# Kernel tuning notes

Measured on AMD Instinct MI355X. Metric: run time of the kernel, lower is better.

The kernel has to match this reference:

```python
import jax, jax.numpy as jnp
import numpy as np

B_, L_, D_, E_, N_, DT_, K_ = 2, 1024, 1024, 2048, 16, 64, 4
EPS = 1e-5


def setup_inputs() -> dict:
    key = jax.random.key(0)
    ks = jax.random.split(key, 16)
    s = lambda *sh: 1.0 / np.sqrt(sh[-1])
    return {
        "resid": jax.random.normal(ks[0], (B_, L_, D_), jnp.float32),
        "norm_w": jnp.ones((D_,), jnp.float32),
        "skip_w": jax.random.normal(ks[1], (E_, D_), jnp.float32) * s(E_, D_),
        "in_w": jax.random.normal(ks[2], (E_, D_), jnp.float32) * s(E_, D_),
        "conv_w": jax.random.normal(ks[3], (E_, K_), jnp.float32) * s(E_, K_),
        "conv_b": jax.random.normal(ks[4], (E_,), jnp.float32) * 0.1,
        "wd1": jax.random.normal(ks[5], (DT_, E_), jnp.float32) * s(DT_, E_),
        "wd2": jax.random.normal(ks[6], (E_, DT_), jnp.float32) * s(E_, DT_),
        "wd2_b": jax.random.normal(ks[7], (E_,), jnp.float32) * 0.1,
        "wb": jax.random.normal(ks[8], (N_, E_), jnp.float32) * s(N_, E_),
        "wc": jax.random.normal(ks[9], (N_, E_), jnp.float32) * s(N_, E_),
        "A_log": jnp.log(jax.random.uniform(ks[10], (E_, N_), jnp.float32, 0.5, 4.0)),
        "W_D": jnp.ones((E_,), jnp.float32),
        "out_w": jax.random.normal(ks[11], (D_, E_), jnp.float32) * s(D_, E_),
    }


def _forward(resid, norm_w, skip_w, in_w, conv_w, conv_b, wd1, wd2, wd2_b,
             wb, wc, A_log, W_D, out_w):
    B, L, D = resid.shape
    E, N = A_log.shape
    K = conv_w.shape[-1]
    # RMSNorm
    xn = resid * jax.lax.rsqrt(jnp.mean(resid * resid, -1, keepdims=True) + EPS) * norm_w
    skip = jnp.einsum('bld,ed->ble', xn, skip_w)
    x = jnp.einsum('bld,ed->ble', xn, in_w)
    # causal depthwise conv1d (torch pads both sides by K-1, output cut to [:L])
    xp = jnp.pad(x, ((0, 0), (K - 1, 0), (0, 0)))
    conv = conv_b + sum(xp[:, k:k + L, :] * conv_w[:, k] for k in range(K))
    x = jax.nn.silu(conv)  # [B,L,E] ssm input
    # input-dependent projections
    delta = jax.nn.softplus(jnp.einsum('ble,re->blr', x, wd1) @ wd2.T + wd2_b)  # [B,L,E]
    Bt = jnp.einsum('ble,ne->bln', x, wb)  # [B,L,N]
    Ct = jnp.einsum('ble,ne->bln', x, wc)  # [B,L,N]
    A = -jnp.exp(A_log)  # [E,N]

    def step(h, inp):
        dt, b_t, c_t, x_t = inp  # [B,E],[B,N],[B,N],[B,E]
        A_bar = jnp.exp(dt[:, :, None] * A)          # [B,E,N]
        h = A_bar * h + (dt * x_t)[:, :, None] * b_t[:, None, :]
        y = jnp.einsum('ben,bn->be', h, c_t)
        return h, y

    h0 = jnp.zeros((B, E, N), x.dtype)
    xs = (delta.transpose(1, 0, 2), Bt.transpose(1, 0, 2),
          Ct.transpose(1, 0, 2), x.transpose(1, 0, 2))
    _, y = jax.lax.scan(step, h0, xs)
    y = y.transpose(1, 0, 2)  # [B,L,E]
    y = y + x * W_D
    y = y * jax.nn.silu(skip)
    y = jnp.einsum('ble,de->bld', y, out_w)
    return resid + y


def reference(resid, norm_w, skip_w, in_w, conv_w, conv_b, wd1, wd2, wd2_b,
              wb, wc, A_log, W_D, out_w):
    return _forward(resid, norm_w, skip_w, in_w, conv_w, conv_b, wd1, wd2,
                    wd2_b, wb, wc, A_log, W_D, out_w)
```

## Files before the change

### kernel.cpp

```cpp
#include <hip/hip_runtime.h>
#include <cstdint>

typedef unsigned short u16;
typedef float f32x4 __attribute__((ext_vector_type(4)));
typedef __bf16 bf16x8 __attribute__((ext_vector_type(8)));
typedef u16 u16x8 __attribute__((ext_vector_type(8)));

__device__ __forceinline__ u16 f2bf(float f) {
  uint32_t u = __float_as_uint(f);
  u += 0x7fffu + ((u >> 16) & 1u);
  return (u16)(u >> 16);
}
__device__ __forceinline__ float bf2f(u16 s) {
  return __uint_as_float(((uint32_t)s) << 16);
}

__device__ __forceinline__ void ld16(const u16* g, u16* l) {
  auto* gp = reinterpret_cast<const __attribute__((address_space(1))) u16*>(
      reinterpret_cast<uintptr_t>(g));
  auto* lp = reinterpret_cast<__attribute__((address_space(3))) u16*>(
      static_cast<uint32_t>(reinterpret_cast<uintptr_t>(l)));
  __builtin_amdgcn_global_load_lds(gp, lp, 16, 0, 0);
}

__device__ __forceinline__ f32x4 mfma16(u16x8 a, u16x8 b, f32x4 c) {
  return __builtin_amdgcn_mfma_f32_16x16x32_bf16(
      __builtin_bit_cast(bf16x8, a), __builtin_bit_cast(bf16x8, b), c, 0, 0, 0);
}

__device__ __forceinline__ float sigmoidf_(float x) { return 1.f / (1.f + __expf(-x)); }
__device__ __forceinline__ float siluf_(float x) { return x * sigmoidf_(x); }
__device__ __forceinline__ float softplusf_(float x) {
  return fmaxf(x, 0.f) + log1pf(__expf(-fabsf(x)));
}

#define PACK_TOT 6651904
__global__ __launch_bounds__(256) void pack_rms_kernel(
    const float* __restrict__ skip_w, const float* __restrict__ in_w,
    const float* __restrict__ out_w, const float* __restrict__ wd2,
    const float* __restrict__ wd1, const float* __restrict__ wb,
    const float* __restrict__ wc, const float* __restrict__ A_log,
    u16* __restrict__ skipw_bf, u16* __restrict__ inw_bf, u16* __restrict__ outw_bf,
    u16* __restrict__ wd2_bf, u16* __restrict__ w96, float* __restrict__ Aneg,
    const float* __restrict__ resid, const float* __restrict__ norm_w,
    u16* __restrict__ xn_bf) {
  int t = threadIdx.x;
  if (blockIdx.x >= 1024) {
    int row = blockIdx.x - 1024;
    const float4* xr = (const float4*)(resid + (size_t)row * 1024);
    float4 v = xr[t];
    float ss = v.x * v.x + v.y * v.y + v.z * v.z + v.w * v.w;
    for (int o = 32; o > 0; o >>= 1) ss += __shfl_xor(ss, o);
    __shared__ float wsum[4];
    if ((t & 63) == 0) wsum[t >> 6] = ss;
    __syncthreads();
    float tot = wsum[0] + wsum[1] + wsum[2] + wsum[3];
    float rs = rsqrtf(tot * (1.0f / 1024.0f) + 1e-5f);
    float4 wv = ((const float4*)norm_w)[t];
    uint2 pk;
    pk.x = (uint32_t)f2bf(v.x * rs * wv.x) | ((uint32_t)f2bf(v.y * rs * wv.y) << 16);
    pk.y = (uint32_t)f2bf(v.z * rs * wv.z) | ((uint32_t)f2bf(v.w * rs * wv.w) << 16);
    ((uint2*)xn_bf)[row * 256 + t] = pk;
    return;
  }
  const int stride = 1024 * 256;
  for (int i = blockIdx.x * 256 + t; i < PACK_TOT; i += stride) {
    int j = i;
    if (j < 2097152) { skipw_bf[j] = f2bf(skip_w[j]); continue; } j -= 2097152;
    if (j < 2097152) { inw_bf[j] = f2bf(in_w[j]); continue; } j -= 2097152;
    if (j < 2097152) { outw_bf[j] = f2bf(out_w[j]); continue; } j -= 2097152;
    if (j < 131072)  { wd2_bf[j] = f2bf(wd2[j]); continue; } j -= 131072;
    if (j < 131072)  { w96[j] = f2bf(wd1[j]); continue; } j -= 131072;
    if (j < 32768)   { w96[131072 + j] = f2bf(wb[j]); continue; } j -= 32768;
    if (j < 32768)   { w96[163840 + j] = f2bf(wc[j]); continue; } j -= 32768;
    Aneg[j] = -__expf(A_log[j]);
  }
}

template <int BM, int BN, int BK, int EPI>
__global__ __launch_bounds__(256) void gemm_bt(
    const u16* __restrict__ A, const u16* __restrict__ B0, const u16* __restrict__ B1,
    int M, int N, int K, int Nsplit,
    void* __restrict__ C0, void* __restrict__ C1,
    const float* __restrict__ addsrc) {
  constexpr int TM = BM / 32, TN = BN / 32;
  constexpr int KC = BK / 8;
  __shared__ __align__(16) u16 sA[BM * BK];
  __shared__ __align__(16) u16 sB[BN * BK];
  const int t = threadIdx.x;
  const int lane = t & 63, wid = t >> 6;
  const int wm = wid >> 1, wn = wid & 1;
  const int mBase = blockIdx.y * BM;
  const int nBase = blockIdx.x * BN;
  const bool hi = (nBase >= Nsplit);
  const u16* Bp = hi ? B1 : B0;
  const int nB0 = nBase - (hi ? Nsplit : 0);
  const int col = lane & 15, quad = lane >> 4;

  f32x4 acc[TM][TN];
#pragma unroll
  for (int i = 0; i < TM; ++i)
#pragma unroll
    for (int j = 0; j < TN; ++j) acc[i][j] = f32x4{0.f, 0.f, 0.f, 0.f};

  for (int k0 = 0; k0 < K; k0 += BK) {
#pragma unroll
    for (int c = t; c < BM * KC; c += 256) {
      int row = c / KC, j = c % KC;
      int k8 = ((j + row) & (KC - 1)) * 8;
      ld16(A + (size_t)(mBase + row) * K + k0 + k8, &sA[c * 8]);
    }
#pragma unroll
    for (int c = t; c < BN * KC; c += 256) {
      int row = c / KC, j = c % KC;
      int k8 = ((j + row) & (KC - 1)) * 8;
      ld16(Bp + (size_t)(nB0 + row) * K + k0 + k8, &sB[c * 8]);
    }
    __syncthreads();
#pragma unroll
    for (int kk = 0; kk < BK / 32; ++kk) {
      u16x8 af[TM], bfv[TN];
#pragma unroll
      for (int i = 0; i < TM; ++i) {
        int rowA = wm * (BM / 2) + i * 16 + col;
        af[i] = *(const u16x8*)&sA[rowA * BK + (((kk * 4 + quad) - rowA) & (KC - 1)) * 8];
      }
#pragma unroll
      for (int j = 0; j < TN; ++j) {
        int rowB = wn * (BN / 2) + j * 16 + col;
        bfv[j] = *(const u16x8*)&sB[rowB * BK + (((kk * 4 + quad) - rowB) & (KC - 1)) * 8];
      }
#pragma unroll
      for (int i = 0; i < TM; ++i)
#pragma unroll
        for (int j = 0; j < TN; ++j) acc[i][j] = mfma16(af[i], bfv[j], acc[i][j]);
    }
    __syncthreads();
  }

#pragma unroll
  for (int i = 0; i < TM; ++i) {
#pragma unroll
    for (int j = 0; j < TN; ++j) {
#pragma unroll
      for (int r = 0; r < 4; ++r) {
        int gm = mBase + wm * (BM / 2) + i * 16 + quad * 4 + r;
        int gn = nBase + wn * (BN / 2) + j * 16 + col;
        float v = acc[i][j][r];
        if (EPI == 0) {
          if (gn < Nsplit)
            ((u16*)C0)[(size_t)gm * Nsplit + gn] = f2bf(v);
          else
            ((u16*)C1)[(size_t)gm * (N - Nsplit) + (gn - Nsplit)] = f2bf(v);
        } else {
          ((float*)C0)[(size_t)gm * N + gn] = addsrc[(size_t)gm * N + gn] + v;
        }
      }
    }
  }
}

__global__ __launch_bounds__(256) void conv_skinny_kernel(
    const u16* __restrict__ xin_bf, const float* __restrict__ conv_w,
    const float* __restrict__ conv_b, u16* __restrict__ xconv_bf,
    const u16* __restrict__ w96, float* __restrict__ dbc) {
  constexpr int PAD = 264;
  __shared__ __align__(16) u16 sA[64 * PAD];
  __shared__ __align__(16) u16 sB[96 * 128];
  const int t = threadIdx.x, lane = t & 63, w = t >> 6;
  const int mBase = blockIdx.x * 64;
  const int e0 = blockIdx.y * 256;

  {
    const int ep = (t & 127) * 2;
    const int strip = t >> 7;
    const int ms = mBase + strip * 32;
    const int l0 = ms & 1023;
    const uint32_t* xr = (const uint32_t*)xin_bf;
    size_t base = ((size_t)ms * 2048 + e0 + ep) >> 1;
    int eg = e0 + ep;
    float4 w0 = ((const float4*)conv_w)[eg];
    float4 w1 = ((const float4*)conv_w)[eg + 1];
    float b0 = conv_b[eg], b1 = conv_b[eg + 1];
    uint32_t u;
    u = (l0 >= 1) ? xr[base - 1024] : 0u;
    float h10 = bf2f((u16)u), h11 = bf2f((u16)(u >> 16));
    u = (l0 >= 2) ? xr[base - 2048] : 0u;
    float h20 = bf2f((u16)u), h21 = bf2f((u16)(u >> 16));
    u = (l0 >= 3) ? xr[base - 3072] : 0u;
    float h30 = bf2f((u16)u), h31 = bf2f((u16)(u >> 16));
#pragma unroll 4
    for (int r = 0; r < 32; ++r) {
      uint32_t ux = xr[base + (size_t)r * 1024];
      float x0 = bf2f((u16)ux), x1 = bf2f((u16)(ux >> 16));
      float a0 = b0 + w0.w * x0 + w0.z * h10 + w0.y * h20 + w0.x * h30;
      float a1 = b1 + w1.w * x1 + w1.z * h11 + w1.y * h21 + w1.x * h31;
      a0 = siluf_(a0); a1 = siluf_(a1);
      uint32_t pk = (uint32_t)f2bf(a0) | ((uint32_t)f2bf(a1) << 16);
      ((uint32_t*)xconv_bf)[base + (size_t)r * 1024] = pk;
      *(uint32_t*)&sA[(strip * 32 + r) * PAD + ep] = pk;
      h30 = h20; h31 = h21; h20 = h10; h21 = h11; h10 = x0; h11 = x1;
    }
  }
  for (int c = t; c < 96 * 16; c += 256) {
    int row = c >> 4, j = c & 15;
    int k8 = ((j + row) & 15) * 8;
    ld16(w96 + (size_t)row * 2048 + e0 + k8, &sB[c * 8]);
  }
  __syncthreads();
  const int col = lane & 15, quad = lane >> 4;
  const int rowA = w * 16 + col;
  f32x4 acc[6];
#pragma unroll
  for (int j = 0; j < 6; ++j) acc[j] = f32x4{0.f, 0.f, 0.f, 0.f};
#pragma unroll
  for (int kk = 0; kk < 4; ++kk) {
    u16x8 af = *(const u16x8*)&sA[rowA * PAD + kk * 32 + quad * 8];
#pragma unroll
    for (int j = 0; j < 6; ++j) {
      int rowB = j * 16 + col;
      u16x8 bfv = *(const u16x8*)&sB[rowB * 128 + (((kk * 4 + quad) - rowB) & 15) * 8];
      acc[j] = mfma16(af, bfv, acc[j]);
    }
  }
  __syncthreads();
  for (int c = t; c < 96 * 16; c += 256) {
    int row = c >> 4, j = c & 15;
    int k8 = ((j + row) & 15) * 8;
    ld16(w96 + (size_t)row * 2048 + e0 + 128 + k8, &sB[c * 8]);
  }
  __syncthreads();
#pragma unroll
  for (int kk = 4; kk < 8; ++kk) {
    u16x8 af = *(const u16x8*)&sA[rowA * PAD + kk * 32 + quad * 8];
#pragma unroll
    for (int j = 0; j < 6; ++j) {
      int rowB = j * 16 + col;
      u16x8 bfv = *(const u16x8*)&sB[rowB * 128 + ((((kk - 4) * 4 + quad) - rowB) & 15) * 8];
      acc[j] = mfma16(af, bfv, acc[j]);
    }
  }
#pragma unroll
  for (int j = 0; j < 6; ++j)
#pragma unroll
    for (int r = 0; r < 4; ++r) {
      int gm = mBase + w * 16 + quad * 4 + r;
      int gn = j * 16 + col;
      atomicAdd(&dbc[gm * 96 + gn], acc[j][r]);
    }
}

__device__ __forceinline__ void delta_tile(
    const float* __restrict__ dbc, const u16* __restrict__ wd2_bf,
    const float* __restrict__ wd2_b, int m0, int e0,
    u16* sD1, float* sDT, float* sBC) {
  const int t = threadIdx.x;
  for (int i = t; i < 2048; i += 256)
    sD1[i] = f2bf(dbc[(m0 + (i >> 6)) * 96 + (i & 63)]);
  for (int j = t; j < 1024; j += 256)
    sBC[j] = dbc[(m0 + (j >> 5)) * 96 + 64 + (j & 31)];
  __syncthreads();
  const int lane = t & 63, wid = t >> 6;
  const int col = lane & 15, quad = lane >> 4;
  const int mt = wid & 1, ntB = (wid >> 1) * 8;
  u16x8 afr0 = *(const u16x8*)&sD1[(mt * 16 + col) * 64 + quad * 8];
  u16x8 afr1 = *(const u16x8*)&sD1[(mt * 16 + col) * 64 + 32 + quad * 8];
#pragma unroll
  for (int jj = 0; jj < 8; ++jj) {
    int ecol = (ntB + jj) * 16 + col;
    int erow = e0 + ecol;
    u16x8 b0 = *(const u16x8*)&wd2_bf[(size_t)erow * 64 + quad * 8];
    u16x8 b1 = *(const u16x8*)&wd2_bf[(size_t)erow * 64 + 32 + quad * 8];
    f32x4 dacc = f32x4{0.f, 0.f, 0.f, 0.f};
    dacc = mfma16(afr0, b0, dacc);
    dacc = mfma16(afr1, b1, dacc);
    float bias = wd2_b[erow];
#pragma unroll
    for (int r = 0; r < 4; ++r)
      sDT[(mt * 16 + quad * 4 + r) * 260 + ecol] = softplusf_(dacc[r] + bias);
  }
  __syncthreads();
}

__global__ __launch_bounds__(256) void scan1_kernel(
    const float* __restrict__ dbc, const u16* __restrict__ wd2_bf,
    const float* __restrict__ wd2_b, const u16* __restrict__ xconv_bf,
    const float* __restrict__ Aneg, float* __restrict__ hloc,
    float* __restrict__ Ssum) {
  __shared__ __align__(16) float sDT[32 * 260];
  __shared__ __align__(16) u16 sD1[32 * 64];
  __shared__ float sBC[1024];
  const int t = threadIdx.x;
  const int eb = blockIdx.x, c = blockIdx.y, b = blockIdx.z;
  const int e0 = eb * 256;
  const int m0 = b * 1024 + c * 32;
  delta_tile(dbc, wd2_bf, wd2_b, m0, e0, sD1, sDT, sBC);
  const int e = e0 + t;
  float Ar[16], h[16];
#pragma unroll
  for (int n = 0; n < 16; ++n) { Ar[n] = Aneg[e * 16 + n]; h[n] = 0.f; }
  float S = 0.f;
  for (int l = 0; l < 32; ++l) {
    size_t m = (size_t)(m0 + l) * 2048 + e;
    float dt = sDT[l * 260 + t];
    float xv = bf2f(xconv_bf[m]);
    S += dt;
    float dx = dt * xv;
    const float* bl = &sBC[l * 32];
#pragma unroll
    for (int n = 0; n < 16; ++n) h[n] = __expf(dt * Ar[n]) * h[n] + dx * bl[n];
  }
  size_t base = ((size_t)(b * 32 + c) * 2048 + e) * 16;
#pragma unroll
  for (int n = 0; n < 16; ++n) hloc[base + n] = h[n];
  Ssum[(b * 32 + c) * 2048 + e] = S;
}

__global__ __launch_bounds__(256) void combine_kernel(
    const float* __restrict__ Aneg, const float* __restrict__ Ssum,
    float* __restrict__ hloc) {
  int tid = blockIdx.x * 256 + threadIdx.x;
  int b = tid >> 15, r = tid & 32767;
  int e = r >> 4;
  float a = Aneg[r];
  float h = 0.f;
  for (int c = 0; c < 32; ++c) {
    size_t base = (size_t)(b * 32 + c) * 32768 + r;
    float hl = hloc[base];
    float S = Ssum[(b * 32 + c) * 2048 + e];
    hloc[base] = h;
    h = __expf(a * S) * h + hl;
  }
}

__global__ __launch_bounds__(256) void scan2_kernel(
    const float* __restrict__ dbc, const u16* __restrict__ wd2_bf,
    const float* __restrict__ wd2_b, const u16* __restrict__ xconv_bf,
    const float* __restrict__ Aneg, const float* __restrict__ hloc,
    const u16* __restrict__ skip_bf, const float* __restrict__ W_D,
    u16* __restrict__ yfin_bf) {
  __shared__ __align__(16) float sDT[32 * 260];
  __shared__ __align__(16) u16 sD1[32 * 64];
  __shared__ float sBC[1024];
  const int t = threadIdx.x;
  const int eb = blockIdx.x, c = blockIdx.y, b = blockIdx.z;
  const int e0 = eb * 256;
  const int m0 = b * 1024 + c * 32;
  delta_tile(dbc, wd2_bf, wd2_b, m0, e0, sD1, sDT, sBC);
  const int e = e0 + t;
  float Ar[16], h[16];
  size_t hbase = ((size_t)(b * 32 + c) * 2048 + e) * 16;
#pragma unroll
  for (int n = 0; n < 16; ++n) { Ar[n] = Aneg[e * 16 + n]; h[n] = hloc[hbase + n]; }
  float wd = W_D[e];
  for (int l = 0; l < 32; ++l) {
    size_t m = (size_t)(m0 + l) * 2048 + e;
    float dt = sDT[l * 260 + t];
    float xv = bf2f(xconv_bf[m]);
    float dx = dt * xv;
    const float* bl = &sBC[l * 32];
    float y = 0.f;
#pragma unroll
    for (int n = 0; n < 16; ++n) {
      h[n] = __expf(dt * Ar[n]) * h[n] + dx * bl[n];
      y += h[n] * bl[16 + n];
    }
    float yv = y + xv * wd;
    float sk = bf2f(skip_bf[m]);
    yv *= sk * sigmoidf_(sk);
    yfin_bf[m] = f2bf(yv);
  }
}

extern "C" void kernel_launch(void* const* d_in, const int* in_sizes, int n_in,
                              void* d_out, int out_size, void* d_ws, size_t ws_size,
                              hipStream_t stream) {
  (void)in_sizes; (void)n_in; (void)out_size; (void)ws_size;
  const float* resid  = (const float*)d_in[0];
  const float* norm_w = (const float*)d_in[1];
  const float* skip_w = (const float*)d_in[2];
  const float* in_w   = (const float*)d_in[3];
  const float* conv_w = (const float*)d_in[4];
  const float* conv_b = (const float*)d_in[5];
  const float* wd1    = (const float*)d_in[6];
  const float* wd2    = (const float*)d_in[7];
  const float* wd2_b  = (const float*)d_in[8];
  const float* wb     = (const float*)d_in[9];
  const float* wc     = (const float*)d_in[10];
  const float* A_log  = (const float*)d_in[11];
  const float* W_D    = (const float*)d_in[12];
  const float* out_w  = (const float*)d_in[13];

  char* p = (char*)d_ws;
  u16*   skipw_bf = (u16*)(p + 0);
  u16*   inw_bf   = (u16*)(p + 4194304);
  u16*   outw_bf  = (u16*)(p + 8388608);
  u16*   wd2_bf   = (u16*)(p + 12582912);
  u16*   w96      = (u16*)(p + 12845056);
  float* Aneg     = (float*)(p + 13238272);
  u16*   xn_bf    = (u16*)(p + 13369344);
  u16*   skip_bf  = (u16*)(p + 17563648);
  u16*   xin_bf   = (u16*)(p + 25952256);
  u16*   xconv_bf = (u16*)(p + 34340864);
  float* dbc      = (float*)(p + 42729472);
  u16*   yfin_bf  = (u16*)(p + 43515904);
  float* hloc     = (float*)(p + 51904512);
  float* Ssum     = (float*)(p + 60293120);

  hipMemsetAsync((void*)dbc, 0, 2048 * 96 * sizeof(float), stream);
  pack_rms_kernel<<<3072, 256, 0, stream>>>(
      skip_w, in_w, out_w, wd2, wd1, wb, wc, A_log,
      skipw_bf, inw_bf, outw_bf, wd2_bf, w96, Aneg,
      resid, norm_w, xn_bf);
  gemm_bt<128, 128, 64, 0><<<dim3(32, 16), 256, 0, stream>>>(
      xn_bf, skipw_bf, inw_bf, 2048, 4096, 1024, 2048,
      (void*)skip_bf, (void*)xin_bf, nullptr);
  conv_skinny_kernel<<<dim3(32, 8), 256, 0, stream>>>(
      xin_bf, conv_w, conv_b, xconv_bf, w96, dbc);
  scan1_kernel<<<dim3(8, 32, 2), 256, 0, stream>>>(
      dbc, wd2_bf, wd2_b, xconv_bf, Aneg, hloc, Ssum);
  combine_kernel<<<256, 256, 0, stream>>>(Aneg, Ssum, hloc);
  scan2_kernel<<<dim3(8, 32, 2), 256, 0, stream>>>(
      dbc, wd2_bf, wd2_b, xconv_bf, Aneg, hloc, skip_bf, W_D, yfin_bf);
  gemm_bt<64, 64, 128, 2><<<dim3(16, 32), 256, 0, stream>>>(
      yfin_bf, outw_bf, outw_bf, 2048, 1024, 2048, 1024,
      (void*)d_out, nullptr, resid);
}
```

Before: 236.3 us.

## Split-K output GEMM with atomics, smaller tiles, and more blocks for conv and combine

The out-projection GEMM is split along K into two halves that accumulate into the output with atomicAdd. The output is pre-seeded with the residual through a device memcpy. The input GEMM uses 128x64 tiles with launch_bounds occupancy 4, giving more blocks. The conv kernel processes 128 channels per block so twice as many blocks launch, and the combine kernel prefetches the next chunk and uses smaller blocks. The aim is to fill more CUs on small grids, at the cost of atomic traffic, non-deterministic summation order and an extra memcpy.

```diff
diff --git a/kernel.cpp b/kernel.cpp
--- a/kernel.cpp
+++ b/kernel.cpp
@@ -78,11 +78,10 @@
 }
 
 template <int BM, int BN, int BK, int EPI>
-__global__ __launch_bounds__(256) void gemm_bt(
+__global__ __launch_bounds__(256, 4) void gemm_bt(
     const u16* __restrict__ A, const u16* __restrict__ B0, const u16* __restrict__ B1,
-    int M, int N, int K, int Nsplit,
-    void* __restrict__ C0, void* __restrict__ C1,
-    const float* __restrict__ addsrc) {
+    int N, int K, int Kld, int mTiles, int Nsplit,
+    void* __restrict__ C0, void* __restrict__ C1) {
   constexpr int TM = BM / 32, TN = BN / 32;
   constexpr int KC = BK / 8;
   __shared__ __align__(16) u16 sA[BM * BK];
@@ -90,7 +89,9 @@
   const int t = threadIdx.x;
   const int lane = t & 63, wid = t >> 6;
   const int wm = wid >> 1, wn = wid & 1;
-  const int mBase = blockIdx.y * BM;
+  const int by = blockIdx.y & (mTiles - 1);
+  const int kOff = (blockIdx.y / mTiles) * K;
+  const int mBase = by * BM;
   const int nBase = blockIdx.x * BN;
   const bool hi = (nBase >= Nsplit);
   const u16* Bp = hi ? B1 : B0;
@@ -103,18 +104,18 @@
 #pragma unroll
     for (int j = 0; j < TN; ++j) acc[i][j] = f32x4{0.f, 0.f, 0.f, 0.f};
 
-  for (int k0 = 0; k0 < K; k0 += BK) {
+  for (int k0 = kOff; k0 < kOff + K; k0 += BK) {
 #pragma unroll
     for (int c = t; c < BM * KC; c += 256) {
       int row = c / KC, j = c % KC;
       int k8 = ((j + row) & (KC - 1)) * 8;
-      ld16(A + (size_t)(mBase + row) * K + k0 + k8, &sA[c * 8]);
+      ld16(A + (size_t)(mBase + row) * Kld + k0 + k8, &sA[c * 8]);
     }
 #pragma unroll
     for (int c = t; c < BN * KC; c += 256) {
       int row = c / KC, j = c % KC;
       int k8 = ((j + row) & (KC - 1)) * 8;
-      ld16(Bp + (size_t)(nB0 + row) * K + k0 + k8, &sB[c * 8]);
+      ld16(Bp + (size_t)(nB0 + row) * Kld + k0 + k8, &sB[c * 8]);
     }
     __syncthreads();
 #pragma unroll
@@ -153,7 +154,7 @@
           else
             ((u16*)C1)[(size_t)gm * (N - Nsplit) + (gn - Nsplit)] = f2bf(v);
         } else {
-          ((float*)C0)[(size_t)gm * N + gn] = addsrc[(size_t)gm * N + gn] + v;
+          atomicAdd(&((float*)C0)[(size_t)gm * N + gn], v);
         }
       }
     }
@@ -164,17 +165,17 @@
     const u16* __restrict__ xin_bf, const float* __restrict__ conv_w,
     const float* __restrict__ conv_b, u16* __restrict__ xconv_bf,
     const u16* __restrict__ w96, float* __restrict__ dbc) {
-  constexpr int PAD = 264;
+  constexpr int PAD = 136;
   __shared__ __align__(16) u16 sA[64 * PAD];
   __shared__ __align__(16) u16 sB[96 * 128];
   const int t = threadIdx.x, lane = t & 63, w = t >> 6;
   const int mBase = blockIdx.x * 64;
-  const int e0 = blockIdx.y * 256;
+  const int e0 = blockIdx.y * 128;
 
   {
-    const int ep = (t & 127) * 2;
-    const int strip = t >> 7;
-    const int ms = mBase + strip * 32;
+    const int ep = (t & 63) * 2;
+    const int strip = t >> 6;
+    const int ms = mBase + strip * 16;
     const int l0 = ms & 1023;
     const uint32_t* xr = (const uint32_t*)xin_bf;
     size_t base = ((size_t)ms * 2048 + e0 + ep) >> 1;
@@ -190,7 +191,7 @@
     u = (l0 >= 3) ? xr[base - 3072] : 0u;
     float h30 = bf2f((u16)u), h31 = bf2f((u16)(u >> 16));
 #pragma unroll 4
-    for (int r = 0; r < 32; ++r) {
+    for (int r = 0; r < 16; ++r) {
       uint32_t ux = xr[base + (size_t)r * 1024];
       float x0 = bf2f((u16)ux), x1 = bf2f((u16)(ux >> 16));
       float a0 = b0 + w0.w * x0 + w0.z * h10 + w0.y * h20 + w0.x * h30;
@@ -198,7 +199,7 @@
       a0 = siluf_(a0); a1 = siluf_(a1);
       uint32_t pk = (uint32_t)f2bf(a0) | ((uint32_t)f2bf(a1) << 16);
       ((uint32_t*)xconv_bf)[base + (size_t)r * 1024] = pk;
-      *(uint32_t*)&sA[(strip * 32 + r) * PAD + ep] = pk;
+      *(uint32_t*)&sA[(strip * 16 + r) * PAD + ep] = pk;
       h30 = h20; h31 = h21; h20 = h10; h21 = h11; h10 = x0; h11 = x1;
     }
   }
@@ -220,23 +221,6 @@
     for (int j = 0; j < 6; ++j) {
       int rowB = j * 16 + col;
       u16x8 bfv = *(const u16x8*)&sB[rowB * 128 + (((kk * 4 + quad) - rowB) & 15) * 8];
-      acc[j] = mfma16(af, bfv, acc[j]);
-    }
-  }
-  __syncthreads();
-  for (int c = t; c < 96 * 16; c += 256) {
-    int row = c >> 4, j = c & 15;
-    int k8 = ((j + row) & 15) * 8;
-    ld16(w96 + (size_t)row * 2048 + e0 + 128 + k8, &sB[c * 8]);
-  }
-  __syncthreads();
-#pragma unroll
-  for (int kk = 4; kk < 8; ++kk) {
-    u16x8 af = *(const u16x8*)&sA[rowA * PAD + kk * 32 + quad * 8];
-#pragma unroll
-    for (int j = 0; j < 6; ++j) {
-      int rowB = j * 16 + col;
-      u16x8 bfv = *(const u16x8*)&sB[rowB * 128 + ((((kk - 4) * 4 + quad) - rowB) & 15) * 8];
       acc[j] = mfma16(af, bfv, acc[j]);
     }
   }
@@ -316,20 +300,25 @@
   Ssum[(b * 32 + c) * 2048 + e] = S;
 }
 
-__global__ __launch_bounds__(256) void combine_kernel(
+__global__ __launch_bounds__(128) void combine_kernel(
     const float* __restrict__ Aneg, const float* __restrict__ Ssum,
     float* __restrict__ hloc) {
-  int tid = blockIdx.x * 256 + threadIdx.x;
+  int tid = blockIdx.x * 128 + threadIdx.x;
   int b = tid >> 15, r = tid & 32767;
   int e = r >> 4;
   float a = Aneg[r];
   float h = 0.f;
+  float hl = hloc[(size_t)(b * 32) * 32768 + r];
+  float S = Ssum[(b * 32) * 2048 + e];
   for (int c = 0; c < 32; ++c) {
-    size_t base = (size_t)(b * 32 + c) * 32768 + r;
-    float hl = hloc[base];
-    float S = Ssum[(b * 32 + c) * 2048 + e];
-    hloc[base] = h;
+    float hl2 = 0.f, S2 = 0.f;
+    if (c < 31) {
+      hl2 = hloc[(size_t)(b * 32 + c + 1) * 32768 + r];
+      S2 = Ssum[(b * 32 + c + 1) * 2048 + e];
+    }
+    hloc[(size_t)(b * 32 + c) * 32768 + r] = h;
     h = __expf(a * S) * h + hl;
+    hl = hl2; S = S2;
   }
 }
 
@@ -408,21 +397,23 @@
   float* Ssum     = (float*)(p + 60293120);
 
   hipMemsetAsync((void*)dbc, 0, 2048 * 96 * sizeof(float), stream);
+  hipMemcpyAsync(d_out, (const void*)resid, 2048 * 1024 * sizeof(float),
+                 hipMemcpyDeviceToDevice, stream);
   pack_rms_kernel<<<3072, 256, 0, stream>>>(
       skip_w, in_w, out_w, wd2, wd1, wb, wc, A_log,
       skipw_bf, inw_bf, outw_bf, wd2_bf, w96, Aneg,
       resid, norm_w, xn_bf);
-  gemm_bt<128, 128, 64, 0><<<dim3(32, 16), 256, 0, stream>>>(
-      xn_bf, skipw_bf, inw_bf, 2048, 4096, 1024, 2048,
-      (void*)skip_bf, (void*)xin_bf, nullptr);
-  conv_skinny_kernel<<<dim3(32, 8), 256, 0, stream>>>(
+  gemm_bt<128, 64, 64, 0><<<dim3(64, 16), 256, 0, stream>>>(
+      xn_bf, skipw_bf, inw_bf, 4096, 1024, 1024, 16, 2048,
+      (void*)skip_bf, (void*)xin_bf);
+  conv_skinny_kernel<<<dim3(32, 16), 256, 0, stream>>>(
       xin_bf, conv_w, conv_b, xconv_bf, w96, dbc);
   scan1_kernel<<<dim3(8, 32, 2), 256, 0, stream>>>(
       dbc, wd2_bf, wd2_b, xconv_bf, Aneg, hloc, Ssum);
-  combine_kernel<<<256, 256, 0, stream>>>(Aneg, Ssum, hloc);
+  combine_kernel<<<512, 128, 0, stream>>>(Aneg, Ssum, hloc);
   scan2_kernel<<<dim3(8, 32, 2), 256, 0, stream>>>(
       dbc, wd2_bf, wd2_b, xconv_bf, Aneg, hloc, skip_bf, W_D, yfin_bf);
-  gemm_bt<64, 64, 128, 2><<<dim3(16, 32), 256, 0, stream>>>(
-      yfin_bf, outw_bf, outw_bf, 2048, 1024, 2048, 1024,
-      (void*)d_out, nullptr, resid);
-}
+  gemm_bt<128, 64, 64, 3><<<dim3(16, 32), 256, 0, stream>>>(
+      yfin_bf, outw_bf, outw_bf, 1024, 1024, 2048, 16, 1024,
+      (void*)d_out, nullptr);
+}
```

After: 241.4 us. 2.1% more time.
